# Performance work log

Measured on AMD Instinct MI355X. Metric: run time of the kernel, lower is better.

Reference implementation:

```python
import math
import jax, jax.numpy as jnp
import numpy as np

B, C, D = 4, 1024, 2048
N_EXP, TOP_K, CAP_F = 8, 2, 1.25


def setup_inputs() -> dict:
    key = jax.random.key(0)
    k1, k2, k3, k4 = jax.random.split(key, 4)
    x = jax.random.normal(k1, (B, C, D), dtype=jnp.float32)
    noise = jax.random.normal(k2, (B, C, N_EXP), dtype=jnp.float32)
    w_g = jax.random.normal(k3, (N_EXP, D), dtype=jnp.float32) * 0.02
    w_noise = jax.random.normal(k4, (N_EXP, D), dtype=jnp.float32) * 0.02
    return {"x": x, "noise": noise, "w_g": w_g, "w_noise": w_noise}


def reference(x, noise, w_g, w_noise):
    b, c, d = x.shape
    T = b * c  # num_tokens
    E, k = w_g.shape[0], TOP_K

    # gating logits with noisy top-k (noise eps passed in explicitly)
    logits = jnp.einsum('bcd,ed->bce', x, w_g)
    logits = logits + jax.nn.softplus(jnp.einsum('bcd,ed->bce', x, w_noise)) * noise

    top_vals, top_idx = jax.lax.top_k(logits, k)  # (B,C,k)

    # scatter top-k logits into -inf tensor then softmax == mask non-topk to -inf
    onehot_k = jax.nn.one_hot(top_idx, E, dtype=jnp.int32)  # (B,C,k,E)
    topk_mask = onehot_k.sum(axis=-2) > 0                   # (B,C,E)
    router_probs = jax.nn.softmax(jnp.where(topk_mask, logits, -jnp.inf), axis=-1)

    cap = math.floor(k * CAP_F * T / E)
    cap += cap % 2

    # (k, T, E) expert assignment mask
    exp_mask = onehot_k.reshape(T, k, E).transpose(1, 0, 2)
    # position-in-expert rank via cumulative sum over (k*T, E)
    exp_rank = jnp.cumsum(exp_mask.reshape(k * T, E), axis=0) - 1
    exp_rank = exp_rank.reshape(k, T, E)
    exp_mask = exp_mask * (exp_rank < cap).astype(jnp.int32)
    rank = jnp.sum(exp_mask * exp_rank, axis=-1)  # (k, T) int

    probs_flat = router_probs.reshape(T, E)[None]          # (1,T,E)
    w = exp_mask.astype(x.dtype) * probs_flat              # (k,T,E)
    rank_oh = jax.nn.one_hot(rank, cap, dtype=x.dtype)     # (k,T,cap)
    # combine weights: (T, E, cap)
    exp_weights = jnp.einsum('kte,ktc->tec', w, rank_oh)
    exp_mask_out = exp_weights != 0                        # bool (T,E,cap)

    x_flat = x.reshape(T, d)
    # dense one-hot dispatch matmul: (E, cap, T) @ (T, d)
    expert_batches = jnp.einsum('tec,td->ecd', exp_mask_out.astype(x.dtype), x_flat)
    return exp_weights, exp_mask_out, expert_batches
```

## Files before the change

### kernel.cpp

```cpp
#include <hip/hip_runtime.h>

#define T_TOKENS 4096
#define D_DIM    2048
#define NEXP     8
#define CAP      1280
#define NSLOTS   (NEXP * CAP)

#define GATE_TPB   512
#define GATE_TPW   2
#define GATE_TPBK  16
#define GATE_BLOCKS (T_TOKENS / GATE_TPBK)
#define GCHUNK     512
#define GCHUNK4    (GCHUNK / 4)
#define NCHUNK     (D_DIM / GCHUNK)

typedef float f32x4 __attribute__((ext_vector_type(4)));

__device__ __forceinline__ float dot4(f32x4 a, f32x4 b) {
    return a.x * b.x + a.y * b.y + a.z * b.z + a.w * b.w;
}

__global__ void gating_kernel(const float* __restrict__ x,
                              const float* __restrict__ noise,
                              const float* __restrict__ w_g,
                              const float* __restrict__ w_noise,
                              int*   __restrict__ top_idx,
                              float* __restrict__ top_prob)
{
    __shared__ f32x4 s_wg[NEXP][GCHUNK4];
    __shared__ f32x4 s_wn[NEXP][GCHUNK4];

    const int w    = threadIdx.x >> 6;
    const int lane = threadIdx.x & 63;
    const int t0   = blockIdx.x * GATE_TPBK + w * GATE_TPW;

    const f32x4* x0 = reinterpret_cast<const f32x4*>(x + (size_t)t0 * D_DIM);
    const f32x4* x1 = reinterpret_cast<const f32x4*>(x + (size_t)(t0 + 1) * D_DIM);

    float accg[GATE_TPW][NEXP];
    float accn[GATE_TPW][NEXP];
#pragma unroll
    for (int τ = 0; τ < GATE_TPW; ++τ)
#pragma unroll
        for (int e = 0; e < NEXP; ++e) { accg[τ][e] = 0.f; accn[τ][e] = 0.f; }

    for (int ch = 0; ch < NCHUNK; ++ch) {
        const int base4 = ch * GCHUNK4;
#pragma unroll
        for (int j = threadIdx.x; j < NEXP * GCHUNK4; j += GATE_TPB) {
            const int e = j / GCHUNK4, c = j % GCHUNK4;
            s_wg[e][c] = reinterpret_cast<const f32x4*>(w_g     + (size_t)e * D_DIM)[base4 + c];
            s_wn[e][c] = reinterpret_cast<const f32x4*>(w_noise + (size_t)e * D_DIM)[base4 + c];
        }
        __syncthreads();

#pragma unroll
        for (int i = 0; i < GCHUNK4 / 64; ++i) {
            const int c = i * 64 + lane;
            const f32x4 xv0 = x0[base4 + c];
            const f32x4 xv1 = x1[base4 + c];
#pragma unroll
            for (int e = 0; e < NEXP; ++e) {
                const f32x4 g = s_wg[e][c];
                const f32x4 n = s_wn[e][c];
                accg[0][e] += dot4(xv0, g);
                accg[1][e] += dot4(xv1, g);
                accn[0][e] += dot4(xv0, n);
                accn[1][e] += dot4(xv1, n);
            }
        }
        __syncthreads();
    }

#pragma unroll
    for (int τ = 0; τ < GATE_TPW; ++τ)
#pragma unroll
        for (int e = 0; e < NEXP; ++e) {
            float vg = accg[τ][e], vn = accn[τ][e];
#pragma unroll
            for (int off = 32; off > 0; off >>= 1) {
                vg += __shfl_down(vg, off, 64);
                vn += __shfl_down(vn, off, 64);
            }
            accg[τ][e] = vg; accn[τ][e] = vn;
        }

    if (lane == 0) {
#pragma unroll
        for (int τ = 0; τ < GATE_TPW; ++τ) {
            const int t = t0 + τ;
            float logit[NEXP];
#pragma unroll
            for (int e = 0; e < NEXP; ++e) {
                const float z = accn[τ][e];
                const float sp = fmaxf(z, 0.f) + log1pf(expf(-fabsf(z)));
                logit[e] = accg[τ][e] + sp * noise[(size_t)t * NEXP + e];
            }
            int i0 = 0; float v0 = logit[0];
#pragma unroll
            for (int e = 1; e < NEXP; ++e)
                if (logit[e] > v0) { v0 = logit[e]; i0 = e; }
            int i1 = -1; float v1 = -3.402823466e38f;
#pragma unroll
            for (int e = 0; e < NEXP; ++e)
                if (e != i0 && logit[e] > v1) { v1 = logit[e]; i1 = e; }
            const float e1  = expf(v1 - v0);
            const float inv = 1.f / (1.f + e1);
            top_idx[t]            = i0;
            top_idx[T_TOKENS + t] = i1;
            top_prob[t]            = inv;
            top_prob[T_TOKENS + t] = e1 * inv;
        }
    }
}

__global__ void scan_scatter_kernel(const int*   __restrict__ top_idx,
                                    const float* __restrict__ top_prob,
                                    int*   __restrict__ slot_token,
                                    float* __restrict__ exp_weights,
                                    float* __restrict__ exp_mask)
{
    __shared__ int sidx[2 * T_TOKENS];
    __shared__ int scnt[8];

    const int e    = blockIdx.x;
    const int w    = threadIdx.x >> 6;
    const int lane = threadIdx.x & 63;

    for (int i = threadIdx.x; i < 2 * T_TOKENS; i += 512)
        sidx[i] = top_idx[i];
    for (int r = threadIdx.x; r < CAP; r += 512)
        slot_token[e * CAP + r] = -1;
    __syncthreads();

    int cnt = 0;
#pragma unroll
    for (int c = 0; c < 16; ++c) {
        const int i = (w * 16 + c) * 64 + lane;
        cnt += __popcll(__ballot(sidx[i] == e));
    }
    if (lane == 0) scnt[w] = cnt;
    __syncthreads();

    int base = 0;
#pragma unroll
    for (int j = 0; j < 8; ++j) if (j < w) base += scnt[j];

#pragma unroll
    for (int c = 0; c < 16; ++c) {
        const int i = (w * 16 + c) * 64 + lane;
        const bool match = (sidx[i] == e);
        const unsigned long long m = __ballot(match);
        if (match) {
            const int r = base + __popcll(m & ((1ull << lane) - 1ull));
            if (r < CAP) {
                slot_token[e * CAP + r] = i;
                const int t = i & (T_TOKENS - 1);
                const float wgt = top_prob[i];
                const size_t off = (size_t)t * NSLOTS + e * CAP + r;
                exp_weights[off] = wgt;
                exp_mask[off]    = (wgt != 0.f) ? 1.f : 0.f;
            }
        }
        base += __popcll(m);
    }
}

__global__ void batches_kernel(const float* __restrict__ x,
                               const int*   __restrict__ slot_token,
                               float* __restrict__ expert_batches)
{
    const int slot = blockIdx.x;
    const int i = slot_token[slot];
    f32x4* dst = reinterpret_cast<f32x4*>(expert_batches + (size_t)slot * D_DIM);

    if (i >= 0) {
        const int t = i & (T_TOKENS - 1);
        const f32x4* src = reinterpret_cast<const f32x4*>(x + (size_t)t * D_DIM);
#pragma unroll
        for (int c = threadIdx.x; c < D_DIM / 4; c += 256)
            dst[c] = src[c];
    } else {
        const f32x4 z = {0.f, 0.f, 0.f, 0.f};
#pragma unroll
        for (int c = threadIdx.x; c < D_DIM / 4; c += 256)
            dst[c] = z;
    }
}

extern "C" void kernel_launch(void* const* d_in, const int* in_sizes, int n_in,
                              void* d_out, int out_size, void* d_ws, size_t ws_size,
                              hipStream_t stream)
{
    const float* x       = (const float*)d_in[0];
    const float* noise   = (const float*)d_in[1];
    const float* w_g     = (const float*)d_in[2];
    const float* w_noise = (const float*)d_in[3];

    float* out = (float*)d_out;
    const size_t n_ew = (size_t)T_TOKENS * NEXP * CAP;
    float* exp_weights    = out;
    float* exp_mask       = out + n_ew;
    float* expert_batches = out + 2 * n_ew;

    int*   top_idx    = (int*)d_ws;
    float* top_prob   = (float*)((char*)d_ws + 2 * T_TOKENS * 4);
    int*   slot_token = (int*)((char*)d_ws + 4 * T_TOKENS * 4);

    (void)hipMemsetAsync(out, 0, 2 * n_ew * sizeof(float), stream);

    gating_kernel<<<GATE_BLOCKS, GATE_TPB, 0, stream>>>(x, noise, w_g, w_noise,
                                                        top_idx, top_prob);
    scan_scatter_kernel<<<NEXP, 512, 0, stream>>>(top_idx, top_prob, slot_token,
                                                  exp_weights, exp_mask);
    batches_kernel<<<NSLOTS, 256, 0, stream>>>(x, slot_token, expert_batches);
}
```

Measured before the change: 135.3 us.

## Fuse zero-fill and scatter into one dense writer kernel with nontemporal stores

Removes the separate memset of the two large (T, E*cap) outputs and the sparse scatter. The scan kernel now records only per-assignment ranks and slot tokens. A single writer kernel then emits every output row densely: each weight or mask row is built in registers with its two nonzero entries, and the expert_batches rows are copied in the same launch. All stores use nontemporal global_store_dwordx4 to avoid cache pollution. The aim is to cut a launch and the scattered read-modify traffic, in exchange for per-element compare logic and inline asm stores.

```diff
diff --git a/kernel.cpp b/kernel.cpp
--- a/kernel.cpp
+++ b/kernel.cpp
@@ -1,4 +1,5 @@
 #include <hip/hip_runtime.h>
+#include <stdint.h>
 
 #define T_TOKENS 4096
 #define D_DIM    2048
@@ -20,6 +21,11 @@
     return a.x * b.x + a.y * b.y + a.z * b.z + a.w * b.w;
 }
 
+__device__ __forceinline__ void stream_store(f32x4* p, f32x4 v) {
+    asm volatile("global_store_dwordx4 %0, %1, off sc0 sc1 nt"
+                 :: "v"(p), "v"(v) : "memory");
+}
+
 __global__ void gating_kernel(const float* __restrict__ x,
                               const float* __restrict__ noise,
                               const float* __restrict__ w_g,
@@ -40,9 +46,9 @@
     float accg[GATE_TPW][NEXP];
     float accn[GATE_TPW][NEXP];
 #pragma unroll
-    for (int τ = 0; τ < GATE_TPW; ++τ)
-#pragma unroll
-        for (int e = 0; e < NEXP; ++e) { accg[τ][e] = 0.f; accn[τ][e] = 0.f; }
+    for (int q = 0; q < GATE_TPW; ++q)
+#pragma unroll
+        for (int e = 0; e < NEXP; ++e) { accg[q][e] = 0.f; accn[q][e] = 0.f; }
 
     for (int ch = 0; ch < NCHUNK; ++ch) {
         const int base4 = ch * GCHUNK4;
@@ -73,28 +79,28 @@
     }
 
 #pragma unroll
-    for (int τ = 0; τ < GATE_TPW; ++τ)
+    for (int q = 0; q < GATE_TPW; ++q)
 #pragma unroll
         for (int e = 0; e < NEXP; ++e) {
-            float vg = accg[τ][e], vn = accn[τ][e];
+            float vg = accg[q][e], vn = accn[q][e];
 #pragma unroll
             for (int off = 32; off > 0; off >>= 1) {
                 vg += __shfl_down(vg, off, 64);
                 vn += __shfl_down(vn, off, 64);
             }
-            accg[τ][e] = vg; accn[τ][e] = vn;
+            accg[q][e] = vg; accn[q][e] = vn;
         }
 
     if (lane == 0) {
 #pragma unroll
-        for (int τ = 0; τ < GATE_TPW; ++τ) {
-            const int t = t0 + τ;
+        for (int q = 0; q < GATE_TPW; ++q) {
+            const int t = t0 + q;
             float logit[NEXP];
 #pragma unroll
             for (int e = 0; e < NEXP; ++e) {
-                const float z = accn[τ][e];
+                const float z = accn[q][e];
                 const float sp = fmaxf(z, 0.f) + log1pf(expf(-fabsf(z)));
-                logit[e] = accg[τ][e] + sp * noise[(size_t)t * NEXP + e];
+                logit[e] = accg[q][e] + sp * noise[(size_t)t * NEXP + e];
             }
             int i0 = 0; float v0 = logit[0];
 #pragma unroll
@@ -114,11 +120,9 @@
     }
 }
 
-__global__ void scan_scatter_kernel(const int*   __restrict__ top_idx,
-                                    const float* __restrict__ top_prob,
-                                    int*   __restrict__ slot_token,
-                                    float* __restrict__ exp_weights,
-                                    float* __restrict__ exp_mask)
+__global__ void scan_kernel(const int* __restrict__ top_idx,
+                            int* __restrict__ rank,
+                            int* __restrict__ slot_token)
 {
     __shared__ int sidx[2 * T_TOKENS];
     __shared__ int scnt[8];
@@ -153,38 +157,72 @@
         const unsigned long long m = __ballot(match);
         if (match) {
             const int r = base + __popcll(m & ((1ull << lane) - 1ull));
-            if (r < CAP) {
-                slot_token[e * CAP + r] = i;
-                const int t = i & (T_TOKENS - 1);
-                const float wgt = top_prob[i];
-                const size_t off = (size_t)t * NSLOTS + e * CAP + r;
-                exp_weights[off] = wgt;
-                exp_mask[off]    = (wgt != 0.f) ? 1.f : 0.f;
-            }
+            const bool keep = (r < CAP);
+            rank[i] = keep ? r : -1;
+            if (keep) slot_token[e * CAP + r] = i;
         }
         base += __popcll(m);
     }
 }
 
-__global__ void batches_kernel(const float* __restrict__ x,
-                               const int*   __restrict__ slot_token,
-                               float* __restrict__ expert_batches)
-{
-    const int slot = blockIdx.x;
-    const int i = slot_token[slot];
-    f32x4* dst = reinterpret_cast<f32x4*>(expert_batches + (size_t)slot * D_DIM);
-
-    if (i >= 0) {
-        const int t = i & (T_TOKENS - 1);
-        const f32x4* src = reinterpret_cast<const f32x4*>(x + (size_t)t * D_DIM);
-#pragma unroll
-        for (int c = threadIdx.x; c < D_DIM / 4; c += 256)
-            dst[c] = src[c];
-    } else {
-        const f32x4 z = {0.f, 0.f, 0.f, 0.f};
-#pragma unroll
-        for (int c = threadIdx.x; c < D_DIM / 4; c += 256)
-            dst[c] = z;
+__global__ void writer_kernel(const float* __restrict__ x,
+                              const int*   __restrict__ top_idx,
+                              const float* __restrict__ top_prob,
+                              const int*   __restrict__ rank,
+                              const int*   __restrict__ slot_token,
+                              float* __restrict__ exp_weights,
+                              float* __restrict__ exp_mask,
+                              float* __restrict__ expert_batches)
+{
+    const int bid = blockIdx.x;
+
+    if (bid < NSLOTS) {
+        const int slot = bid;
+        const int i = slot_token[slot];
+        f32x4* dst = reinterpret_cast<f32x4*>(expert_batches + (size_t)slot * D_DIM);
+
+        if (i >= 0) {
+            const int t = i & (T_TOKENS - 1);
+            const f32x4* src = reinterpret_cast<const f32x4*>(x + (size_t)t * D_DIM);
+#pragma unroll
+            for (int c = threadIdx.x; c < D_DIM / 4; c += 256)
+                stream_store(dst + c, src[c]);
+        } else {
+            const f32x4 z = {0.f, 0.f, 0.f, 0.f};
+#pragma unroll
+            for (int c = threadIdx.x; c < D_DIM / 4; c += 256)
+                stream_store(dst + c, z);
+        }
+        return;
+    }
+
+    const bool is_mask = (bid >= NSLOTS + T_TOKENS);
+    const int t = bid - NSLOTS - (is_mask ? T_TOKENS : 0);
+
+    const int e0 = top_idx[t];
+    const int e1 = top_idx[T_TOKENS + t];
+    const int r0 = rank[t];
+    const int r1 = rank[T_TOKENS + t];
+    const float w0 = top_prob[t];
+    const float w1 = top_prob[T_TOKENS + t];
+
+    const int p0 = (r0 >= 0) ? (e0 * CAP + r0) : -1;
+    const int p1 = (r1 >= 0) ? (e1 * CAP + r1) : -1;
+    const float v0 = is_mask ? ((w0 != 0.f) ? 1.f : 0.f) : w0;
+    const float v1 = is_mask ? ((w1 != 0.f) ? 1.f : 0.f) : w1;
+
+    float* base = is_mask ? exp_mask : exp_weights;
+    f32x4* out = reinterpret_cast<f32x4*>(base + (size_t)t * NSLOTS);
+
+#pragma unroll
+    for (int f = threadIdx.x; f < NSLOTS / 4; f += 256) {
+        const int b = 4 * f;
+        f32x4 v;
+        v.x = (b     == p0) ? v0 : (b     == p1) ? v1 : 0.f;
+        v.y = (b + 1 == p0) ? v0 : (b + 1 == p1) ? v1 : 0.f;
+        v.z = (b + 2 == p0) ? v0 : (b + 2 == p1) ? v1 : 0.f;
+        v.w = (b + 3 == p0) ? v0 : (b + 3 == p1) ? v1 : 0.f;
+        stream_store(out + f, v);
     }
 }
 
@@ -205,13 +243,13 @@
 
     int*   top_idx    = (int*)d_ws;
     float* top_prob   = (float*)((char*)d_ws + 2 * T_TOKENS * 4);
-    int*   slot_token = (int*)((char*)d_ws + 4 * T_TOKENS * 4);
-
-    (void)hipMemsetAsync(out, 0, 2 * n_ew * sizeof(float), stream);
+    int*   rank       = (int*)((char*)d_ws + 4 * T_TOKENS * 4);
+    int*   slot_token = (int*)((char*)d_ws + 6 * T_TOKENS * 4);
 
     gating_kernel<<<GATE_BLOCKS, GATE_TPB, 0, stream>>>(x, noise, w_g, w_noise,
                                                         top_idx, top_prob);
-    scan_scatter_kernel<<<NEXP, 512, 0, stream>>>(top_idx, top_prob, slot_token,
-                                                  exp_weights, exp_mask);
-    batches_kernel<<<NSLOTS, 256, 0, stream>>>(x, slot_token, expert_batches);
-}
+    scan_kernel<<<NEXP, 512, 0, stream>>>(top_idx, rank, slot_token);
+    writer_kernel<<<NSLOTS + 2 * T_TOKENS, 256, 0, stream>>>(
+        x, top_idx, top_prob, rank, slot_token,
+        exp_weights, exp_mask, expert_batches);
+}
```

Measured after the change: 131.2 us. 1.03x faster.
